# Kernel optimization log

Measured on AMD Instinct MI355X. Metric: run time of the kernel, lower is better.

## Reference

```python
import jax, jax.numpy as jnp
import numpy as np

B, D, H = 16384, 1024, 16
HD = D // H
EPS = 1e-5


def setup_inputs() -> dict:
    key = jax.random.key(0)
    ks = jax.random.split(key, 16)
    w = lambda k, shape: jax.random.normal(k, shape, jnp.float32) * 0.02
    return {
        "img_emb": jax.random.normal(ks[0], (B, D), jnp.float32),
        "txt_emb": jax.random.normal(ks[1], (B, D), jnp.float32),
        "route_choice": jax.random.randint(ks[2], (B,), 0, 3, jnp.int32),
        # gate: Linear(2D -> D) + sigmoid
        "Wg": w(ks[3], (2 * D, D)), "bg": jnp.zeros((D,), jnp.float32),
        # MultiheadAttention in/out projections
        "Wqkv": w(ks[4], (D, 3 * D)), "bqkv": jnp.zeros((3 * D,), jnp.float32),
        "Wo": w(ks[5], (D, D)), "bo": jnp.zeros((D,), jnp.float32),
        # LayerNorm
        "gamma": jnp.ones((D,), jnp.float32), "beta": jnp.zeros((D,), jnp.float32),
        # FFN: Linear(D->4D), GELU, Linear(4D->D)
        "Wf1": w(ks[6], (D, 4 * D)), "bf1": jnp.zeros((4 * D,), jnp.float32),
        "Wf2": w(ks[7], (4 * D, D)), "bf2": jnp.zeros((D,), jnp.float32),
    }


def _layernorm(x, gamma, beta):
    mu = jnp.mean(x, axis=-1, keepdims=True)
    var = jnp.mean(jnp.square(x - mu), axis=-1, keepdims=True)
    return (x - mu) * jax.lax.rsqrt(var + EPS) * gamma + beta


def reference(img_emb, txt_emb, route_choice, Wg, bg, Wqkv, bqkv, Wo, bo,
              gamma, beta, Wf1, bf1, Wf2, bf2):
    # Eval mode: energy_loss = 0, no dropout. Routing choice supplied as int input.
    # Compute the 'full' fusion branch densely, then select per sample.
    ri = jnp.concatenate([img_emb, txt_emb], axis=-1)          # [B, 2D]
    gate = jax.nn.sigmoid(ri @ Wg + bg)                        # [B, D]
    fused = gate * img_emb + (1.0 - gate) * txt_emb            # [B, D]

    x = jnp.stack([img_emb, txt_emb], axis=1)                  # [B, 2, D]
    qkv = x @ Wqkv + bqkv                                      # [B, 2, 3D]
    q, k, v = jnp.split(qkv, 3, axis=-1)
    q = q.reshape(B, 2, H, HD)
    k = k.reshape(B, 2, H, HD)
    v = v.reshape(B, 2, H, HD)
    scores = jnp.einsum("bqhd,bkhd->bhqk", q, k) / np.sqrt(HD) # [B, H, 2, 2]
    attn = jax.nn.softmax(scores, axis=-1)
    ctx = jnp.einsum("bhqk,bkhd->bqhd", attn, v).reshape(B, 2, D)
    attn_out = ctx @ Wo + bo                                   # [B, 2, D]

    fused = fused + attn_out.mean(axis=1)
    fused = _layernorm(fused, gamma, beta)
    full_out = jax.nn.gelu(fused @ Wf1 + bf1, approximate=False) @ Wf2 + bf2

    rc = route_choice[:, None]
    out = jnp.where(rc == 0, img_emb, jnp.where(rc == 1, txt_emb, full_out))
    return out
```

## Files before the change

kernel.cpp:

```cpp
#include <hip/hip_runtime.h>
#include <hip/hip_bf16.h>
#include <math.h>

#define NB 16384
#define DIM 1024
#define CAP 6656
#define MT 52
#define MT2 26

using bf16 = __hip_bfloat16;
typedef __attribute__((ext_vector_type(8))) short short8;
typedef __attribute__((ext_vector_type(4))) short short4v;
typedef __attribute__((ext_vector_type(4))) float float4v;

__device__ __forceinline__ void gl_lds16(const void* g, void* l) {
  __builtin_amdgcn_global_load_lds(
      (const __attribute__((address_space(1))) unsigned int*)g,
      (__attribute__((address_space(3))) unsigned int*)l, 16, 0, 0);
}

__device__ __forceinline__ short f2bf(float x) {
  __hip_bfloat16 h = __float2bfloat16(x);
  return *reinterpret_cast<short*>(&h);
}

__device__ __forceinline__ void swz(int bid, int nN, int& m0, int& n0) {
  int x = bid & 7;
  int r = bid >> 3;
  int nl = nN >> 3;
  int nLoc = r % nl;
  int m = r / nl;
  n0 = (x + 8 * nLoc) * 128;
  m0 = m * 128;
}

__device__ __forceinline__ void swz256(int bid, int nN, int& m0, int& n0) {
  int x = bid & 7;
  int r = bid >> 3;
  int nl = nN >> 3;
  n0 = (x + 8 * (r % nl)) * 256;
  m0 = (r / nl) * 256;
}

__device__ __forceinline__ void stage_unit(const bf16* __restrict__ gbase,
                                           int ld, int kc, bf16* ubase, int t) {
#pragma unroll
  for (int j = 0; j < 2; ++j) {
    int ch = t + j * 512;
    int rg = ch >> 6;
    int q = (ch & 63) * 16;
    q ^= ((q >> 9) & 1) << 5;
    const bf16* src =
        gbase + (size_t)(rg * 16 + (q >> 6)) * ld + kc + ((q & 63) >> 1);
    gl_lds16(src, (void*)(ubase + ((t >> 6) << 9) + j * 4096));
  }
}

template <int MODE>
__global__ __launch_bounds__(512, 2) void gemm256(
    const bf16* __restrict__ A0, const bf16* __restrict__ A1,
    const bf16* __restrict__ B0, const bf16* __restrict__ Bg0,
    const bf16* __restrict__ Bg1, const float* __restrict__ bias0,
    const float* __restrict__ bias1, bf16* __restrict__ O0,
    bf16* __restrict__ O1, float* __restrict__ P,
    const int* __restrict__ cntp) {
  const int cnt = *cntp;
  int bid = blockIdx.x;
  int g = 0, sk = 0, m0, n0;
  if constexpr (MODE == 0) {
    g = bid >= 416;
    bid -= g * 416;
    swz256(bid, 16, m0, n0);
  } else if constexpr (MODE == 1) {
    swz256(bid, 16, m0, n0);
  } else {
    sk = bid / 104;
    int rm = bid % 104;
    m0 = (rm >> 2) * 256;
    n0 = (rm & 3) * 256;
  }
  if (m0 >= ((cnt + 255) & ~255)) return;

  constexpr int LDA = (MODE == 2) ? 4096 : 1024;
  constexpr int LDB = (MODE == 2) ? 4096 : 1024;
  constexpr int NIT = (MODE == 2) ? 16 : 8;
  const int kb = (MODE == 2) ? sk * 2048 : 0;

  const bf16* Ab;
  const bf16* Bt;
  if constexpr (MODE == 0) {
    Ab = (g ? A1 : A0) + (size_t)m0 * LDA;
    Bt = (n0 < 3072) ? B0 + (size_t)n0 * 1024
                     : (g ? Bg1 : Bg0) + (size_t)(n0 - 3072) * 1024;
  } else {
    Ab = A0 + (size_t)m0 * LDA;
    Bt = B0 + (size_t)n0 * LDB;
  }

  alignas(16) __shared__ bf16 lds[4][2][8192];
  const int t = threadIdx.x;
  const int wave = t >> 6, lane = t & 63;
  const int wm = wave >> 2, wn = wave & 3;
  const int r16 = lane & 15, quad = lane >> 4;
  const int aoff = ((r16 * 64 + quad * 16) ^ ((r16 & 8) << 2)) >> 1;

#pragma unroll
  for (int s = 0; s < 3; ++s) {
    stage_unit(Ab, LDA, kb + s * 32, &lds[s][0][0], t);
    stage_unit(Bt, LDB, kb + s * 32, &lds[s][1][0], t);
  }
  asm volatile("s_waitcnt vmcnt(8)" ::: "memory");
  __builtin_amdgcn_s_barrier();

  float4v acc[8][4] = {};
  for (int it = 0; it < NIT; ++it) {
#pragma unroll
    for (int ph = 0; ph < 8; ++ph) {
      const int tau = it * 4 + (ph >> 1);
      const int slot = tau & 3;
      const int mq = ph & 1;
      short8 av[4], bv[4];
      const bf16* aU = &lds[slot][0][0];
      const bf16* bU = &lds[slot][1][0];
#pragma unroll
      for (int mi = 0; mi < 4; ++mi)
        av[mi] = *(const short8*)(aU + (wm * 8 + mq * 4 + mi) * 512 + aoff);
#pragma unroll
      for (int ni = 0; ni < 4; ++ni)
        bv[ni] = *(const short8*)(bU + (wn * 4 + ni) * 512 + aoff);
      if ((ph & 1) == 0) {
        const int sg = tau + 3;
        if (sg < NIT * 4) {
          const int sl = sg & 3;
          stage_unit(Ab, LDA, kb + sg * 32, &lds[sl][0][0], t);
          stage_unit(Bt, LDB, kb + sg * 32, &lds[sl][1][0], t);
        }
      }
      __builtin_amdgcn_s_barrier();
      asm volatile("s_waitcnt lgkmcnt(0)" ::: "memory");
      __builtin_amdgcn_s_setprio(1);
#pragma unroll
      for (int mi = 0; mi < 4; ++mi)
#pragma unroll
        for (int ni = 0; ni < 4; ++ni)
          acc[mq * 4 + mi][ni] = __builtin_amdgcn_mfma_f32_16x16x32_bf16(
              av[mi], bv[ni], acc[mq * 4 + mi][ni], 0, 0, 0);
      __builtin_amdgcn_s_setprio(0);
      if (ph == 3 || ph == 7)
        asm volatile("s_waitcnt vmcnt(4)" ::: "memory");
      __builtin_amdgcn_s_barrier();
    }
  }

  const int colb = n0 + wn * 64 + r16;
  if constexpr (MODE == 2) {
    float* out = P + (size_t)sk * CAP * 1024;
#pragma unroll
    for (int nf = 0; nf < 4; ++nf) {
      int gcol = colb + nf * 16;
#pragma unroll
      for (int mf = 0; mf < 8; ++mf)
#pragma unroll
        for (int r = 0; r < 4; ++r) {
          int grow = m0 + wm * 128 + mf * 16 + quad * 4 + r;
          out[(size_t)grow * 1024 + gcol] = acc[mf][nf][r];
        }
    }
  } else {
    const float* bias = (MODE == 0) ? (g ? bias1 : bias0) : bias0;
    bf16* O = (MODE == 0) ? (g ? O1 : O0) : O0;
    float bvv[4];
#pragma unroll
    for (int nf = 0; nf < 4; ++nf) bvv[nf] = bias[colb + nf * 16];
#pragma unroll
    for (int nf = 0; nf < 4; ++nf) {
      int gcol = colb + nf * 16;
#pragma unroll
      for (int mf = 0; mf < 8; ++mf)
#pragma unroll
        for (int r = 0; r < 4; ++r) {
          int grow = m0 + wm * 128 + mf * 16 + quad * 4 + r;
          float v = acc[mf][nf][r] + bvv[nf];
          if constexpr (MODE == 1)
            v = 0.5f * v * (1.f + erff(v * 0.70710678118654752f));
          O[(size_t)grow * 4096 + gcol] = __float2bfloat16(v);
        }
    }
  }
}

__global__ __launch_bounds__(256) void transpose_cast(
    const float* __restrict__ in, bf16* __restrict__ out, int K, int N) {
  __shared__ float tile[32][33];
  int n0 = blockIdx.x * 32, k0 = blockIdx.y * 32;
  int tx = threadIdx.x, ty = threadIdx.y;
#pragma unroll
  for (int i = 0; i < 32; i += 8)
    tile[ty + i][tx] = in[(size_t)(k0 + ty + i) * N + n0 + tx];
  __syncthreads();
#pragma unroll
  for (int i = 0; i < 32; i += 8)
    out[(size_t)(n0 + ty + i) * K + k0 + tx] = __float2bfloat16(tile[tx][ty + i]);
}

__global__ __launch_bounds__(256) void fill_bias(const float* __restrict__ bqkv,
                                                 const float* __restrict__ bg,
                                                 float* __restrict__ biasA,
                                                 float* __restrict__ biasB) {
  int i = blockIdx.x * 256 + threadIdx.x;
  float qv = (i < 3072) ? bqkv[i] : 0.f;
  biasA[i] = qv;
  biasB[i] = (i < 3072) ? qv : bg[i - 3072];
}

__global__ void zero_cnt(int* cnt) { if (threadIdx.x == 0) *cnt = 0; }

__global__ __launch_bounds__(256) void index_build(const int* __restrict__ route,
                                                   int* __restrict__ cnt,
                                                   int* __restrict__ idx,
                                                   int* __restrict__ pos) {
  int r = blockIdx.x * 256 + threadIdx.x;
  if (r < NB && route[r] == 2) {
    int p = atomicAdd(cnt, 1);
    idx[p] = r;
    pos[r] = p;
  }
}

__global__ __launch_bounds__(256) void gather_cast(
    const float* __restrict__ img, const float* __restrict__ txt,
    const int* __restrict__ cnt, const int* __restrict__ idx,
    bf16* __restrict__ xg, bf16* __restrict__ tg) {
  int n = blockIdx.x;
  if (n >= *cnt) return;
  int r = idx[n];
  int c = threadIdx.x * 4;
  float4 vi = *(const float4*)(img + (size_t)r * DIM + c);
  float4 vt = *(const float4*)(txt + (size_t)r * DIM + c);
  short4v pi, pt;
  pi[0] = f2bf(vi.x); pi[1] = f2bf(vi.y); pi[2] = f2bf(vi.z); pi[3] = f2bf(vi.w);
  pt[0] = f2bf(vt.x); pt[1] = f2bf(vt.y); pt[2] = f2bf(vt.z); pt[3] = f2bf(vt.w);
  *(short4v*)(xg + (size_t)n * DIM + c) = pi;
  *(short4v*)(tg + (size_t)n * DIM + c) = pt;
}

__global__ __launch_bounds__(256) void attn_kernel(const bf16* __restrict__ qx,
                                                   const bf16* __restrict__ tx,
                                                   bf16* __restrict__ cmean,
                                                   const int* __restrict__ cntp) {
  const int cnt = *cntp;
  int gw = blockIdx.x * 4 + (threadIdx.x >> 6);
  int lane = threadIdx.x & 63;
  int n = gw >> 4, h = gw & 15;
  if (n >= ((cnt + 127) & ~127)) return;
  const bf16* b0 = qx + (size_t)n * 4096 + h * 64 + lane;
  const bf16* b1 = tx + (size_t)n * 4096 + h * 64 + lane;
  float q0 = __bfloat162float(b0[0]);
  float k0 = __bfloat162float(b0[1024]);
  float v0 = __bfloat162float(b0[2048]);
  float q1 = __bfloat162float(b1[0]);
  float k1 = __bfloat162float(b1[1024]);
  float v1 = __bfloat162float(b1[2048]);
  float s00 = q0 * k0, s01 = q0 * k1, s10 = q1 * k0, s11 = q1 * k1;
#pragma unroll
  for (int d = 32; d > 0; d >>= 1) {
    s00 += __shfl_xor(s00, d);
    s01 += __shfl_xor(s01, d);
    s10 += __shfl_xor(s10, d);
    s11 += __shfl_xor(s11, d);
  }
  const float sc = 0.125f;
  s00 *= sc; s01 *= sc; s10 *= sc; s11 *= sc;
  float m0 = fmaxf(s00, s01), m1 = fmaxf(s10, s11);
  float e00 = expf(s00 - m0), e01 = expf(s01 - m0);
  float e10 = expf(s10 - m1), e11 = expf(s11 - m1);
  float i0 = 1.f / (e00 + e01), i1 = 1.f / (e10 + e11);
  float c0 = (e00 * i0) * v0 + (e01 * i0) * v1;
  float c1 = (e10 * i1) * v0 + (e11 * i1) * v1;
  cmean[(size_t)n * DIM + h * 64 + lane] = __float2bfloat16(0.5f * (c0 + c1));
}

__global__ __launch_bounds__(256) void wo_z_kernel(
    const float* __restrict__ img, const float* __restrict__ txt,
    const bf16* __restrict__ qx, const bf16* __restrict__ tx,
    const bf16* __restrict__ WoT, const float* __restrict__ bg,
    const float* __restrict__ bo, const bf16* __restrict__ cmean,
    bf16* __restrict__ z, const int* __restrict__ cntp, const int* __restrict__ idx) {
  const int cnt = *cntp;
  int m0, n0;
  swz(blockIdx.x, 8, m0, n0);
  if (m0 >= ((cnt + 127) & ~127)) return;
  alignas(16) __shared__ bf16 sA[128 * 32];
  alignas(16) __shared__ bf16 sB[128 * 32];
  const int t = threadIdx.x;
  const int wave = t >> 6, lane = t & 63;
  const int wm = (wave >> 1) * 64, wn = (wave & 1) * 64;
  const int r16 = lane & 15, quad = lane >> 4;

  float4v acc[4][4] = {};
  for (int k0 = 0; k0 < 1024; k0 += 32) {
    if (k0) __syncthreads();
#pragma unroll
    for (int j = 0; j < 2; ++j) {
      int c = t + j * 256;
      int row = c >> 2;
      int kk = k0 + (c & 3) * 8;
      gl_lds16(WoT + (size_t)(n0 + row) * 1024 + kk, (void*)(sB + j * 2048 + wave * 512));
      gl_lds16(cmean + (size_t)(m0 + row) * 1024 + kk, (void*)(sA + j * 2048 + wave * 512));
    }
    __syncthreads();
    short8 af[4], bfr[4];
#pragma unroll
    for (int i = 0; i < 4; ++i) {
      af[i] = *(const short8*)(sA + (wm + i * 16 + r16) * 32 + quad * 8);
      bfr[i] = *(const short8*)(sB + (wn + i * 16 + r16) * 32 + quad * 8);
    }
#pragma unroll
    for (int i = 0; i < 4; ++i)
#pragma unroll
      for (int j = 0; j < 4; ++j)
        acc[i][j] =
            __builtin_amdgcn_mfma_f32_16x16x32_bf16(af[i], bfr[j], acc[i][j], 0, 0, 0);
  }
#pragma unroll
  for (int i = 0; i < 4; ++i)
#pragma unroll
    for (int j = 0; j < 4; ++j) {
      int gcol = n0 + wn + j * 16 + r16;
      float bgv = bg[gcol], bov = bo[gcol];
#pragma unroll
      for (int r = 0; r < 4; ++r) {
        int grow = m0 + wm + i * 16 + quad * 4 + r;
        float zv = 0.f;
        if (grow < cnt) {
          int orow = idx[grow];
          float gp = __bfloat162float(qx[(size_t)grow * 4096 + 3072 + gcol]) +
                     __bfloat162float(tx[(size_t)grow * 4096 + 3072 + gcol]) + bgv;
          float g = 1.f / (1.f + expf(-gp));
          size_t ii = (size_t)orow * DIM + gcol;
          float fm = g * img[ii] + (1.f - g) * txt[ii];
          zv = fm + acc[i][j][r] + bov;
        }
        z[(size_t)grow * DIM + gcol] = __float2bfloat16(zv);
      }
    }
}

__global__ __launch_bounds__(256) void ln_kernel(bf16* __restrict__ z,
                                                 const float* __restrict__ g,
                                                 const float* __restrict__ be,
                                                 const int* __restrict__ cntp) {
  const int cnt = *cntp;
  int b = blockIdx.x, t = threadIdx.x;
  if (b >= ((cnt + 127) & ~127)) return;
  bf16* zr = z + (size_t)b * DIM;
  float v[4];
  float s = 0.f, s2 = 0.f;
#pragma unroll
  for (int i = 0; i < 4; ++i) {
    float x = __bfloat162float(zr[t + 256 * i]);
    v[i] = x; s += x; s2 += x * x;
  }
#pragma unroll
  for (int d = 32; d > 0; d >>= 1) {
    s += __shfl_xor(s, d);
    s2 += __shfl_xor(s2, d);
  }
  __shared__ float rs[4], rs2[4];
  int w = t >> 6, lane = t & 63;
  if (!lane) { rs[w] = s; rs2[w] = s2; }
  __syncthreads();
  s = rs[0] + rs[1] + rs[2] + rs[3];
  s2 = rs2[0] + rs2[1] + rs2[2] + rs2[3];
  float mu = s * (1.f / 1024.f);
  float var = s2 * (1.f / 1024.f) - mu * mu;
  float r = rsqrtf(var + 1e-5f);
#pragma unroll
  for (int i = 0; i < 4; ++i) {
    int c = t + 256 * i;
    zr[c] = __float2bfloat16((v[i] - mu) * r * g[c] + be[c]);
  }
}

__global__ __launch_bounds__(256) void route_out(
    const float* __restrict__ img, const float* __restrict__ txt,
    const int* __restrict__ route, const int* __restrict__ pos,
    const float* __restrict__ parts, const float* __restrict__ bf2,
    float* __restrict__ out) {
  int row = blockIdx.x;
  int rc = route[row];
  int c = threadIdx.x * 4;
  float4 v;
  if (rc == 2) {
    int n = pos[row];
    float4 p0 = *(const float4*)(parts + (size_t)n * 1024 + c);
    float4 p1 = *(const float4*)(parts + (size_t)CAP * 1024 + (size_t)n * 1024 + c);
    float4 b = *(const float4*)(bf2 + c);
    v.x = p0.x + p1.x + b.x;
    v.y = p0.y + p1.y + b.y;
    v.z = p0.z + p1.z + b.z;
    v.w = p0.w + p1.w + b.w;
  } else {
    const float* src = (rc == 0) ? img : txt;
    v = *(const float4*)(src + (size_t)row * DIM + c);
  }
  *(float4*)(out + (size_t)row * DIM + c) = v;
}

extern "C" void kernel_launch(void* const* d_in, const int* in_sizes, int n_in,
                              void* d_out, int out_size, void* d_ws, size_t ws_size,
                              hipStream_t stream) {
  const float* img = (const float*)d_in[0];
  const float* txt = (const float*)d_in[1];
  const int* route = (const int*)d_in[2];
  const float* Wg = (const float*)d_in[3];
  const float* bg = (const float*)d_in[4];
  const float* Wqkv = (const float*)d_in[5];
  const float* bqkv = (const float*)d_in[6];
  const float* Wo = (const float*)d_in[7];
  const float* bo = (const float*)d_in[8];
  const float* gamma = (const float*)d_in[9];
  const float* beta = (const float*)d_in[10];
  const float* Wf1 = (const float*)d_in[11];
  const float* bf1 = (const float*)d_in[12];
  const float* Wf2 = (const float*)d_in[13];
  const float* bf2 = (const float*)d_in[14];

  char* ws = (char*)d_ws;
  size_t off = 0;
  auto alloc = [&](size_t bytes) {
    char* p = ws + off;
    off += (bytes + 255) & ~(size_t)255;
    return p;
  };
  int* cntp = (int*)alloc(256);
  int* idx = (int*)alloc((size_t)NB * 4);
  int* pos = (int*)alloc((size_t)NB * 4);
  float* biasA = (float*)alloc(4096 * 4);
  float* biasB = (float*)alloc(4096 * 4);
  bf16* WqkvT = (bf16*)alloc((size_t)3072 * 1024 * 2);
  bf16* WgTopT = (bf16*)alloc((size_t)1024 * 1024 * 2);
  bf16* WgBotT = (bf16*)alloc((size_t)1024 * 1024 * 2);
  bf16* WoT = (bf16*)alloc((size_t)1024 * 1024 * 2);
  bf16* Wf1T = (bf16*)alloc((size_t)4096 * 1024 * 2);
  bf16* Wf2T = (bf16*)alloc((size_t)1024 * 4096 * 2);
  bf16* xg = (bf16*)alloc((size_t)CAP * 1024 * 2);
  bf16* tg = (bf16*)alloc((size_t)CAP * 1024 * 2);
  bf16* qx = (bf16*)alloc((size_t)CAP * 4096 * 2);
  bf16* tx = (bf16*)alloc((size_t)CAP * 4096 * 2);
  bf16* cmean = (bf16*)alloc((size_t)CAP * 1024 * 2);
  bf16* zb = (bf16*)alloc((size_t)CAP * 1024 * 2);
  bf16* hb = qx;
  float* parts = (float*)tx;

  dim3 tblk(32, 8);
  transpose_cast<<<dim3(3072 / 32, 1024 / 32), tblk, 0, stream>>>(Wqkv, WqkvT, 1024, 3072);
  transpose_cast<<<dim3(1024 / 32, 1024 / 32), tblk, 0, stream>>>(Wg, WgTopT, 1024, 1024);
  transpose_cast<<<dim3(1024 / 32, 1024 / 32), tblk, 0, stream>>>(Wg + 1024 * 1024, WgBotT, 1024, 1024);
  transpose_cast<<<dim3(1024 / 32, 1024 / 32), tblk, 0, stream>>>(Wo, WoT, 1024, 1024);
  transpose_cast<<<dim3(4096 / 32, 1024 / 32), tblk, 0, stream>>>(Wf1, Wf1T, 1024, 4096);
  transpose_cast<<<dim3(1024 / 32, 4096 / 32), tblk, 0, stream>>>(Wf2, Wf2T, 4096, 1024);
  fill_bias<<<16, 256, 0, stream>>>(bqkv, bg, biasA, biasB);

  zero_cnt<<<1, 64, 0, stream>>>(cntp);
  index_build<<<NB / 256, 256, 0, stream>>>(route, cntp, idx, pos);
  gather_cast<<<CAP, 256, 0, stream>>>(img, txt, cntp, idx, xg, tg);

  gemm256<0><<<2 * MT2 * 16, 512, 0, stream>>>(xg, tg, WqkvT, WgTopT, WgBotT,
                                               biasA, biasB, qx, tx, nullptr, cntp);
  attn_kernel<<<CAP * 4, 256, 0, stream>>>(qx, tx, cmean, cntp);
  wo_z_kernel<<<8 * MT, 256, 0, stream>>>(img, txt, qx, tx, WoT, bg, bo, cmean, zb,
                                          cntp, idx);
  ln_kernel<<<CAP, 256, 0, stream>>>(zb, gamma, beta, cntp);
  gemm256<1><<<MT2 * 16, 512, 0, stream>>>(zb, nullptr, Wf1T, nullptr, nullptr,
                                           bf1, nullptr, hb, nullptr, nullptr, cntp);
  gemm256<2><<<MT2 * 4 * 2, 512, 0, stream>>>(hb, nullptr, Wf2T, nullptr, nullptr,
                                              nullptr, nullptr, nullptr, nullptr,
                                              parts, cntp);
  route_out<<<NB, 256, 0, stream>>>(img, txt, route, pos, parts, bf2, (float*)d_out);
}
```

Before: 629.1 us.

## Change LDS swizzle, reuse B fragments across phases, retime stage/wait points

Replaces the LDS bank-conflict swizzle with a new row-based XOR pattern (column chunk xor bits of row) in both staging and fragment reads. B fragments are now loaded once per k-slice and reused across both M halves, reducing LDS reads. Global prefetch is moved to the odd phase and the vmcnt waits are shifted to match, with a full drain on the last iteration. This changes the pipeline timing and risks correctness if the swizzle or wait counts are mismatched.

```diff
diff --git a/kernel.cpp b/kernel.cpp
--- a/kernel.cpp
+++ b/kernel.cpp
@@ -48,10 +48,9 @@
   for (int j = 0; j < 2; ++j) {
     int ch = t + j * 512;
     int rg = ch >> 6;
-    int q = (ch & 63) * 16;
-    q ^= ((q >> 9) & 1) << 5;
-    const bf16* src =
-        gbase + (size_t)(rg * 16 + (q >> 6)) * ld + kc + ((q & 63) >> 1);
+    int rl = (ch >> 2) & 15;
+    int cs = ((ch & 3) * 8) ^ ((rl & 6) << 2);
+    const bf16* src = gbase + (size_t)(rg * 16 + rl) * ld + kc + cs;
     gl_lds16(src, (void*)(ubase + ((t >> 6) << 9) + j * 4096));
   }
 }
@@ -102,33 +101,39 @@
   const int wave = t >> 6, lane = t & 63;
   const int wm = wave >> 2, wn = wave & 3;
   const int r16 = lane & 15, quad = lane >> 4;
-  const int aoff = ((r16 * 64 + quad * 16) ^ ((r16 & 8) << 2)) >> 1;
+  const int xorv = (quad * 8) ^ ((r16 & 6) << 2);
 
 #pragma unroll
   for (int s = 0; s < 3; ++s) {
     stage_unit(Ab, LDA, kb + s * 32, &lds[s][0][0], t);
     stage_unit(Bt, LDB, kb + s * 32, &lds[s][1][0], t);
   }
-  asm volatile("s_waitcnt vmcnt(8)" ::: "memory");
+  asm volatile("s_waitcnt vmcnt(4)" ::: "memory");
   __builtin_amdgcn_s_barrier();
 
   float4v acc[8][4] = {};
   for (int it = 0; it < NIT; ++it) {
+    short8 bv[4];
 #pragma unroll
     for (int ph = 0; ph < 8; ++ph) {
       const int tau = it * 4 + (ph >> 1);
       const int slot = tau & 3;
       const int mq = ph & 1;
-      short8 av[4], bv[4];
       const bf16* aU = &lds[slot][0][0];
       const bf16* bU = &lds[slot][1][0];
-#pragma unroll
-      for (int mi = 0; mi < 4; ++mi)
-        av[mi] = *(const short8*)(aU + (wm * 8 + mq * 4 + mi) * 512 + aoff);
-#pragma unroll
-      for (int ni = 0; ni < 4; ++ni)
-        bv[ni] = *(const short8*)(bU + (wn * 4 + ni) * 512 + aoff);
-      if ((ph & 1) == 0) {
+      short8 av[4];
+#pragma unroll
+      for (int mi = 0; mi < 4; ++mi) {
+        int r = wm * 128 + mq * 64 + mi * 16 + r16;
+        av[mi] = *(const short8*)(aU + r * 32 + xorv);
+      }
+      if (mq == 0) {
+#pragma unroll
+        for (int ni = 0; ni < 4; ++ni) {
+          int r = wn * 64 + ni * 16 + r16;
+          bv[ni] = *(const short8*)(bU + r * 32 + xorv);
+        }
+      } else {
         const int sg = tau + 3;
         if (sg < NIT * 4) {
           const int sl = sg & 3;
@@ -146,8 +151,12 @@
           acc[mq * 4 + mi][ni] = __builtin_amdgcn_mfma_f32_16x16x32_bf16(
               av[mi], bv[ni], acc[mq * 4 + mi][ni], 0, 0, 0);
       __builtin_amdgcn_s_setprio(0);
-      if (ph == 3 || ph == 7)
-        asm volatile("s_waitcnt vmcnt(4)" ::: "memory");
+      if ((ph & 3) == 1) {
+        if (ph == 5 && it == NIT - 1)
+          asm volatile("s_waitcnt vmcnt(0)" ::: "memory");
+        else
+          asm volatile("s_waitcnt vmcnt(4)" ::: "memory");
+      }
       __builtin_amdgcn_s_barrier();
     }
   }
```

New measurement: 628.0 us. Within noise of the previous version (-0.2%).

## Restructure GEMM main loop to one barrier per k-tile with new LDS swizzle

Applied to the files above, without the earlier changes.

Replaces the two-phase-per-tile main loop, which had two barriers per phase, with a single loop over 32-wide k-tiles. Each tile issues the stage-ahead loads, reads all 8 A fragments and 4 B fragments at once, runs 32 MFMAs, and then takes one barrier. The LDS layout becomes a row-major 32-element layout with an XOR swizzle on column chunks, keyed on row bits 1-2, to avoid bank conflicts. The goal is fewer barriers and less synchronisation overhead per MFMA, in exchange for more live registers (8 A fragments) and explicit vmcnt tail handling.

```diff
diff --git a/kernel.cpp b/kernel.cpp
--- a/kernel.cpp
+++ b/kernel.cpp
@@ -48,10 +48,9 @@
   for (int j = 0; j < 2; ++j) {
     int ch = t + j * 512;
     int rg = ch >> 6;
-    int q = (ch & 63) * 16;
-    q ^= ((q >> 9) & 1) << 5;
-    const bf16* src =
-        gbase + (size_t)(rg * 16 + (q >> 6)) * ld + kc + ((q & 63) >> 1);
+    int rl = (ch >> 2) & 15;
+    int cs = ((ch & 3) * 8) ^ ((rl & 6) << 2);
+    const bf16* src = gbase + (size_t)(rg * 16 + rl) * ld + kc + cs;
     gl_lds16(src, (void*)(ubase + ((t >> 6) << 9) + j * 4096));
   }
 }
@@ -83,7 +82,7 @@
 
   constexpr int LDA = (MODE == 2) ? 4096 : 1024;
   constexpr int LDB = (MODE == 2) ? 4096 : 1024;
-  constexpr int NIT = (MODE == 2) ? 16 : 8;
+  constexpr int NK = (MODE == 2) ? 64 : 32;
   const int kb = (MODE == 2) ? sk * 2048 : 0;
 
   const bf16* Ab;
@@ -102,7 +101,7 @@
   const int wave = t >> 6, lane = t & 63;
   const int wm = wave >> 2, wn = wave & 3;
   const int r16 = lane & 15, quad = lane >> 4;
-  const int aoff = ((r16 * 64 + quad * 16) ^ ((r16 & 8) << 2)) >> 1;
+  const int xorv = (quad * 8) ^ ((r16 & 6) << 2);
 
 #pragma unroll
   for (int s = 0; s < 3; ++s) {
@@ -113,43 +112,40 @@
   __builtin_amdgcn_s_barrier();
 
   float4v acc[8][4] = {};
-  for (int it = 0; it < NIT; ++it) {
-#pragma unroll
-    for (int ph = 0; ph < 8; ++ph) {
-      const int tau = it * 4 + (ph >> 1);
-      const int slot = tau & 3;
-      const int mq = ph & 1;
-      short8 av[4], bv[4];
-      const bf16* aU = &lds[slot][0][0];
-      const bf16* bU = &lds[slot][1][0];
-#pragma unroll
-      for (int mi = 0; mi < 4; ++mi)
-        av[mi] = *(const short8*)(aU + (wm * 8 + mq * 4 + mi) * 512 + aoff);
+#pragma unroll 4
+  for (int kt = 0; kt < NK; ++kt) {
+    const int slot = kt & 3;
+    if (kt + 3 < NK) {
+      const int sl = (kt + 3) & 3;
+      stage_unit(Ab, LDA, kb + (kt + 3) * 32, &lds[sl][0][0], t);
+      stage_unit(Bt, LDB, kb + (kt + 3) * 32, &lds[sl][1][0], t);
+    }
+    const bf16* aU = &lds[slot][0][0];
+    const bf16* bU = &lds[slot][1][0];
+    short8 av[8], bv[4];
+#pragma unroll
+    for (int mi = 0; mi < 8; ++mi)
+      av[mi] = *(const short8*)(aU + (wm * 128 + mi * 16 + r16) * 32 + xorv);
+#pragma unroll
+    for (int ni = 0; ni < 4; ++ni)
+      bv[ni] = *(const short8*)(bU + (wn * 64 + ni * 16 + r16) * 32 + xorv);
+    asm volatile("s_waitcnt lgkmcnt(0)" ::: "memory");
+    __builtin_amdgcn_s_setprio(1);
+#pragma unroll
+    for (int mi = 0; mi < 8; ++mi)
 #pragma unroll
       for (int ni = 0; ni < 4; ++ni)
-        bv[ni] = *(const short8*)(bU + (wn * 4 + ni) * 512 + aoff);
-      if ((ph & 1) == 0) {
-        const int sg = tau + 3;
-        if (sg < NIT * 4) {
-          const int sl = sg & 3;
-          stage_unit(Ab, LDA, kb + sg * 32, &lds[sl][0][0], t);
-          stage_unit(Bt, LDB, kb + sg * 32, &lds[sl][1][0], t);
-        }
-      }
-      __builtin_amdgcn_s_barrier();
-      asm volatile("s_waitcnt lgkmcnt(0)" ::: "memory");
-      __builtin_amdgcn_s_setprio(1);
-#pragma unroll
-      for (int mi = 0; mi < 4; ++mi)
-#pragma unroll
-        for (int ni = 0; ni < 4; ++ni)
-          acc[mq * 4 + mi][ni] = __builtin_amdgcn_mfma_f32_16x16x32_bf16(
-              av[mi], bv[ni], acc[mq * 4 + mi][ni], 0, 0, 0);
-      __builtin_amdgcn_s_setprio(0);
-      if (ph == 3 || ph == 7)
-        asm volatile("s_waitcnt vmcnt(4)" ::: "memory");
-      __builtin_amdgcn_s_barrier();
-    }
+        acc[mi][ni] = __builtin_amdgcn_mfma_f32_16x16x32_bf16(
+            av[mi], bv[ni], acc[mi][ni], 0, 0, 0);
+    __builtin_amdgcn_s_setprio(0);
+    if (kt < NK - 3) {
+      asm volatile("s_waitcnt vmcnt(8)" ::: "memory");
+    } else if (kt == NK - 3) {
+      asm volatile("s_waitcnt vmcnt(4)" ::: "memory");
+    } else if (kt == NK - 2) {
+      asm volatile("s_waitcnt vmcnt(0)" ::: "memory");
+    }
+    __builtin_amdgcn_s_barrier();
   }
 
   const int colb = n0 + wn * 64 + r16;
```

Result: no change. 639.1 us (+1.6%).
